# Kernel tuning notes

Hardware: AMD Instinct MI355X
Metric: run time of the kernel (lower is better)

The kernel has to match this reference:

```python
import jax, jax.numpy as jnp
import numpy as np

EMBED_DIM = 768
NUM_HEADS = 12
HEAD_DIM = EMBED_DIM // NUM_HEADS
MAX_WAVELENGTH = 10000.0
ROPE_PERCENT = 0.5


def p_rope(x, positions):
    """Partial RoPE (Gemma-style half-split layout) on x: [BH, S, D]."""
    rope_angles = int(ROPE_PERCENT * HEAD_DIM) // 2
    nope_angles = HEAD_DIM // 2 - rope_angles
    fraction = 2.0 * jnp.arange(rope_angles, dtype=x.dtype) / HEAD_DIM
    timescale = MAX_WAVELENGTH ** fraction
    # infinite timescale => angle 0 => identity rotation for the non-roped dims
    timescale = jnp.concatenate([timescale, jnp.full((nope_angles,), jnp.inf, dtype=x.dtype)])
    sinusoid = positions[:, None] / timescale[None, :]  # [S, D/2]
    sin, cos = jnp.sin(sinusoid), jnp.cos(sinusoid)
    x1, x2 = jnp.split(x, 2, axis=-1)  # each [BH, S, D/2]
    return jnp.concatenate([x1 * cos - x2 * sin, x2 * cos + x1 * sin], axis=-1)


def setup_inputs() -> dict:
    key = jax.random.key(0)
    ks = jax.random.split(key, 9)
    B, T, E = 16, 1024, EMBED_DIM
    s = 0.02
    return {
        "hidden_states": jax.random.normal(ks[0], (B, T, E), jnp.float32),
        "wq": jax.random.normal(ks[1], (E, E), jnp.float32) * s,
        "bq": jax.random.normal(ks[2], (E,), jnp.float32) * s,
        "wk": jax.random.normal(ks[3], (E, E), jnp.float32) * s,
        "bk": jax.random.normal(ks[4], (E,), jnp.float32) * s,
        "wv": jax.random.normal(ks[5], (E, E), jnp.float32) * s,
        "bv": jax.random.normal(ks[6], (E,), jnp.float32) * s,
        "wo": jax.random.normal(ks[7], (E, E), jnp.float32) * s,
        "bo": jax.random.normal(ks[8], (E,), jnp.float32) * s,
    }


def _shape(x, B, S):
    # [B, S, E] -> [B*H, S, head_dim]
    return x.reshape(B, S, NUM_HEADS, HEAD_DIM).transpose(0, 2, 1, 3).reshape(B * NUM_HEADS, S, HEAD_DIM)


def reference(hidden_states, wq, bq, wk, bk, wv, bv, wo, bo):
    B, T, E = hidden_states.shape
    scaling = HEAD_DIM ** -0.5
    # torch nn.Linear: y = x @ W.T + b
    q = (hidden_states @ wq.T + bq) * scaling
    k = hidden_states @ wk.T + bk
    v = hidden_states @ wv.T + bv
    q = _shape(q, B, T)  # [BH, T, D]
    k = _shape(k, B, T)
    v = _shape(v, B, T)
    positions = jnp.arange(T, dtype=hidden_states.dtype)
    k = p_rope(k, positions)
    q = p_rope(q, positions)
    attn = jnp.einsum('bqd,bkd->bqk', q, k)  # [BH, T, T]
    attn = jax.nn.softmax(attn, axis=-1)
    out = jnp.einsum('bqk,bkd->bqd', attn, v)  # [BH, T, D]
    out = out.reshape(B, NUM_HEADS, T, HEAD_DIM).transpose(0, 2, 1, 3).reshape(B, T, E)
    return out @ wo.T + bo
```

## Files before the change

### kernel.cpp

```cpp
#include <hip/hip_runtime.h>
#include <hip/hip_bf16.h>
#include <math.h>

typedef __hip_bfloat16 bf16;
typedef __attribute__((ext_vector_type(8))) __bf16 bf16x8;
typedef __attribute__((ext_vector_type(8))) unsigned short u16x8;
typedef __attribute__((ext_vector_type(4))) float f32x4;
typedef __attribute__((ext_vector_type(16))) float f32x16;
typedef unsigned int u32;
typedef __attribute__((ext_vector_type(4))) unsigned int u32x4;

#define DEVI static __device__ __forceinline__

#define BATCH 16
#define SEQ 1024
#define EMB 768
#define NHEAD 12
#define HDIM 64
#define BHEADS (BATCH * NHEAD)
#define MROWS (BATCH * SEQ)

DEVI f32x4 mfma16x16(bf16x8 a, bf16x8 b, f32x4 c) {
  return __builtin_amdgcn_mfma_f32_16x16x32_bf16(a, b, c, 0, 0, 0);
}
DEVI f32x16 mfma32x32(bf16x8 a, bf16x8 b, f32x16 c) {
  return __builtin_amdgcn_mfma_f32_32x32x16_bf16(a, b, c, 0, 0, 0);
}

DEVI void gload_lds16(const bf16* g, void* lds) {
  __builtin_amdgcn_global_load_lds(
      (const __attribute__((address_space(1))) void*)g,
      (__attribute__((address_space(3))) void*)lds, 16, 0, 0);
}

#if __has_builtin(__builtin_amdgcn_exp2f)
DEVI float fexp2(float x) { return __builtin_amdgcn_exp2f(x); }
#else
DEVI float fexp2(float x) { return exp2f(x); }
#endif

DEVI unsigned short f2bf_bits(float f) {
  bf16 h = __float2bfloat16(f);
  return *reinterpret_cast<unsigned short*>(&h);
}
DEVI u32 pack2(float lo, float hi) {
  return (u32)f2bf_bits(lo) | ((u32)f2bf_bits(hi) << 16);
}

#define N_HS8 (MROWS * EMB / 8)
#define N_W8 (EMB * EMB / 8)

__global__ __launch_bounds__(256) void convert_all_kernel(
    const float* __restrict__ hs, const float* __restrict__ w0,
    const float* __restrict__ w1, const float* __restrict__ w2,
    const float* __restrict__ w3, bf16* __restrict__ dhs,
    bf16* __restrict__ d0, bf16* __restrict__ d1, bf16* __restrict__ d2,
    bf16* __restrict__ d3) {
  int i = blockIdx.x * 256 + threadIdx.x;
  const float* src;
  bf16* dst;
  int j;
  if (i < N_HS8) {
    src = hs; dst = dhs; j = i;
  } else {
    int r = i - N_HS8;
    int which = r / N_W8;
    j = r - which * N_W8;
    src = (which == 0) ? w0 : (which == 1) ? w1 : (which == 2) ? w2 : w3;
    dst = (which == 0) ? d0 : (which == 1) ? d1 : (which == 2) ? d2 : d3;
  }
  const float4* s = (const float4*)src + (long)j * 2;
  float4 a = s[0], b = s[1];
  u16x8 r;
  r[0] = f2bf_bits(a.x); r[1] = f2bf_bits(a.y);
  r[2] = f2bf_bits(a.z); r[3] = f2bf_bits(a.w);
  r[4] = f2bf_bits(b.x); r[5] = f2bf_bits(b.y);
  r[6] = f2bf_bits(b.z); r[7] = f2bf_bits(b.w);
  *(u16x8*)(dst + (long)j * 8) = r;
}

__global__ void rope_table_kernel(float2* __restrict__ tbl) {
  int i = blockIdx.x * 256 + threadIdx.x;
  if (i >= SEQ * 16) return;
  int t = i >> 4;
  int d = i & 15;
  double inv_ts = pow(10000.0, -(double)d / 32.0);
  double ang = (double)t * inv_ts;
  tbl[i] = make_float2((float)cos(ang), (float)sin(ang));
}

DEVI void gemm_core_768(const bf16* __restrict__ A, const bf16* __restrict__ Bt,
                        int rowBase, int colBase, bf16* Asm, bf16* Bsm,
                        f32x4 (&acc)[4][4]) {
  const int K = 768;
  const int NT = 24;
  const int tid = threadIdx.x;
  const int wave = tid >> 6;
  const int lane = tid & 63;
  const int c0 = lane & 15;
  const int khi = lane >> 4;
  const int wm = wave >> 1, wn = wave & 1;
  const int srow = tid >> 2;
  const int scol = ((tid & 3) ^ ((tid >> 3) & 3)) * 8;
  const int sl = (khi ^ ((c0 >> 1) & 3)) * 8;
  const bf16* aG = A + (long)(rowBase + srow) * K + scol;
  const bf16* bG = Bt + (long)(colBase + srow) * K + scol;
  char* aL0 = (char*)Asm + wave * 1024;
  char* aL1 = (char*)Asm + 4096 + wave * 1024;
  char* bL0 = (char*)Bsm + wave * 1024;
  char* bL1 = (char*)Bsm + 4096 + wave * 1024;
  const int stride64 = 64 * K;

#define G_STAGE(boff, kk)                                                    \
  gload_lds16(aG + (kk), aL0 + (boff));                                      \
  gload_lds16(aG + stride64 + (kk), aL1 + (boff));                           \
  gload_lds16(bG + (kk), bL0 + (boff));                                      \
  gload_lds16(bG + stride64 + (kk), bL1 + (boff));

#define G_COMPUTE(be)                                                        \
  {                                                                          \
    bf16x8 af[4], bfr[4];                                                    \
    _Pragma("unroll") for (int m = 0; m < 4; ++m) af[m] =                    \
        *(const bf16x8*)(Asm + (be) + (wm * 64 + m * 16 + c0) * 32 + sl);    \
    _Pragma("unroll") for (int n = 0; n < 4; ++n) bfr[n] =                   \
        *(const bf16x8*)(Bsm + (be) + (wn * 64 + n * 16 + c0) * 32 + sl);    \
    __builtin_amdgcn_s_setprio(1);                                           \
    _Pragma("unroll") for (int m = 0; m < 4; ++m)                            \
      _Pragma("unroll") for (int n = 0; n < 4; ++n)                          \
        acc[m][n] = mfma16x16(af[m], bfr[n], acc[m][n]);                     \
    __builtin_amdgcn_s_setprio(0);                                           \
  }

#define G_PHASE(beElem, sByte, tc)                                           \
  {                                                                          \
    if ((tc) + 1 < NT) {                                                     \
      asm volatile("s_waitcnt vmcnt(4)" ::: "memory");                       \
    } else {                                                                 \
      asm volatile("s_waitcnt vmcnt(0)" ::: "memory");                       \
    }                                                                        \
    __builtin_amdgcn_s_barrier();                                            \
    __builtin_amdgcn_sched_barrier(0);                                       \
    if ((tc) + 2 < NT) { G_STAGE(sByte, ((tc) + 2) * 32); }                  \
    G_COMPUTE(beElem);                                                       \
  }

  G_STAGE(0, 0);
  G_STAGE(8192, 32);

  for (int tt = 0; tt < NT; tt += 3) {
    G_PHASE(0, 16384, tt);
    G_PHASE(4096, 0, tt + 1);
    G_PHASE(8192, 8192, tt + 2);
  }
#undef G_PHASE
#undef G_STAGE
#undef G_COMPUTE
}

__global__ __launch_bounds__(256, 3) void qkv_kernel(
    const bf16* __restrict__ hs,
    const bf16* __restrict__ wq, const float* __restrict__ bq,
    const bf16* __restrict__ wk, const float* __restrict__ bk,
    const bf16* __restrict__ wv, const float* __restrict__ bv,
    const float2* __restrict__ tbl,
    bf16* __restrict__ Qb, bf16* __restrict__ Kb, bf16* __restrict__ Vtb) {
  __shared__ __align__(16) bf16 Asm[3 * 128 * 32];
  __shared__ __align__(16) bf16 Bsm[3 * 128 * 32];
  const int bid = blockIdx.x;
  const int xcd = bid & 7;
  const int i = bid >> 3;
  const int rowtile = xcd * 16 + (i & 15);
  const int yz = i >> 4;
  const int type = yz % 3;
  const int coltile = yz / 3;
  const bf16* W = (type == 0) ? wq : (type == 1) ? wk : wv;
  const float* bias = (type == 0) ? bq : (type == 1) ? bk : bv;
  const int rowBase = rowtile * 128;
  const int colBase = coltile * 128;
  f32x4 acc[4][4] = {};
  gemm_core_768(hs, W, rowBase, colBase, Asm, Bsm, acc);

  const int tid = threadIdx.x;
  const int wave = tid >> 6, lane = tid & 63;
  const int c0 = lane & 15, khi = lane >> 4;
  const int wm = wave >> 1, wn = wave & 1;
  const int colW = colBase + wn * 64;
  const int head = colW >> 6;
  float bb[4];
#pragma unroll
  for (int n = 0; n < 4; ++n) bb[n] = bias[colW + n * 16 + c0];

  const int rW = rowBase + wm * 64;
  const int bIdx = rW >> 10;
  const int bh = bIdx * NHEAD + head;

  if (type == 2) {
#pragma unroll
    for (int m = 0; m < 4; ++m) {
      const int t0 = (rW & 1023) + m * 16 + khi * 4;
#pragma unroll
      for (int n = 0; n < 4; ++n) {
        const int d = n * 16 + c0;
        bf16* vp = Vtb + ((long)bh * HDIM + d) * SEQ + t0;
        ushort4 pk;
        pk.x = f2bf_bits(acc[m][n][0] + bb[n]);
        pk.y = f2bf_bits(acc[m][n][1] + bb[n]);
        pk.z = f2bf_bits(acc[m][n][2] + bb[n]);
        pk.w = f2bf_bits(acc[m][n][3] + bb[n]);
        *(ushort4*)vp = pk;
      }
    }
  } else {
    const float scl = (type == 0) ? 0.125f * 1.44269504f : 1.0f;
    bf16* base = ((type == 0) ? Qb : Kb) + (long)bh * SEQ * HDIM;
#pragma unroll
    for (int m = 0; m < 4; ++m) {
#pragma unroll
      for (int ri = 0; ri < 4; ++ri) {
        const int t = (rW & 1023) + m * 16 + khi * 4 + ri;
        float v0 = (acc[m][0][ri] + bb[0]) * scl;
        float v1 = (acc[m][1][ri] + bb[1]) * scl;
        float v2 = (acc[m][2][ri] + bb[2]) * scl;
        float v3 = (acc[m][3][ri] + bb[3]) * scl;
        const float2 cs = tbl[t * 16 + c0];
        const float r0 = v0 * cs.x - v2 * cs.y;
        const float r2 = v2 * cs.x + v0 * cs.y;
        bf16* qp = base + (long)t * HDIM;
        qp[c0] = __float2bfloat16(r0);
        qp[16 + c0] = __float2bfloat16(v1);
        qp[32 + c0] = __float2bfloat16(r2);
        qp[48 + c0] = __float2bfloat16(v3);
      }
    }
  }
}


DEVI int swoff(int row, int s) {
  return row * 128 + (((s ^ (row & 7)) & 7) << 4);
}

__global__ __launch_bounds__(256, 2) void attn_kernel(
    const bf16* __restrict__ Q, const bf16* __restrict__ K,
    const bf16* __restrict__ Vt, bf16* __restrict__ Ao) {
  __shared__ __align__(16) char smem[4 * 8192];
  const int bid = blockIdx.x;
  const int xcd = bid & 7, idx = bid >> 3;
  const int bh = xcd + ((idx >> 2) << 3);
  const int qt = idx & 3;

  const int tid = threadIdx.x;
  const int lane = tid & 63;
  const int w = tid >> 6;
  const int l31 = lane & 31;
  const int hi = lane >> 5;

  const bf16* Qh = Q + (long)bh * SEQ * HDIM;
  const bf16* Kh = K + (long)bh * SEQ * HDIM;
  const bf16* Vh = Vt + (long)bh * HDIM * SEQ;

  const int qbase = qt * 256 + w * 64;
  bf16x8 qf[2][4];
#pragma unroll
  for (int qn = 0; qn < 2; ++qn)
#pragma unroll
    for (int ks = 0; ks < 4; ++ks)
      qf[qn][ks] = *(const bf16x8*)(Qh + (qbase + qn * 32 + l31) * HDIM +
                                    ks * 16 + hi * 8);

  f32x16 o[2][2] = {};
  float lacc[2] = {0.f, 0.f};

  const int sr = tid >> 3;
  const int sc = tid & 7;

  bf16x8 kr0 = *(const bf16x8*)(Kh + sr * HDIM + sc * 8);
  bf16x8 kr1 = *(const bf16x8*)(Kh + (sr + 32) * HDIM + sc * 8);
  bf16x8 vr0 = *(const bf16x8*)(Vh + sr * SEQ + sc * 8);
  bf16x8 vr1 = *(const bf16x8*)(Vh + (sr + 32) * SEQ + sc * 8);
  *(bf16x8*)(smem + swoff(sr, sc)) = kr0;
  *(bf16x8*)(smem + swoff(sr + 32, sc)) = kr1;
  *(bf16x8*)(smem + 16384 + swoff(sr, sc)) = vr0;
  *(bf16x8*)(smem + 16384 + swoff(sr + 32, sc)) = vr1;
  __syncthreads();

  for (int ct = 0; ct < SEQ / 64; ++ct) {
    const int co = (ct & 1) * 8192;
    const char* Kc = smem + co;
    const char* Vc = smem + 16384 + co;

    if (ct != 15) {
      const int nt = (ct + 1) * 64;
      kr0 = *(const bf16x8*)(Kh + (nt + sr) * HDIM + sc * 8);
      kr1 = *(const bf16x8*)(Kh + (nt + sr + 32) * HDIM + sc * 8);
      vr0 = *(const bf16x8*)(Vh + sr * SEQ + nt + sc * 8);
      vr1 = *(const bf16x8*)(Vh + (sr + 32) * SEQ + nt + sc * 8);
    }

    f32x16 s[2][2] = {};
#pragma unroll
    for (int m = 0; m < 2; ++m)
#pragma unroll
      for (int ks = 0; ks < 4; ++ks) {
        bf16x8 ka = *(const bf16x8*)(Kc + swoff(m * 32 + l31, ks * 2 + hi));
        s[m][0] = mfma32x32(ka, qf[0][ks], s[m][0]);
        s[m][1] = mfma32x32(ka, qf[1][ks], s[m][1]);
      }

    bf16x8 pf[2][4];
#pragma unroll
    for (int qn = 0; qn < 2; ++qn) {
      u32 wds[2][4][2];
#pragma unroll
      for (int m = 0; m < 2; ++m)
#pragma unroll
        for (int b = 0; b < 4; ++b)
#pragma unroll
          for (int pp = 0; pp < 2; ++pp) {
            const float p0 = fexp2(s[m][qn][4 * b + 2 * pp]);
            const float p1 = fexp2(s[m][qn][4 * b + 2 * pp + 1]);
            lacc[qn] += p0 + p1;
            wds[m][b][pp] = pack2(p0, p1);
          }
#pragma unroll
      for (int m = 0; m < 2; ++m)
#pragma unroll
        for (int ts = 0; ts < 2; ++ts) {
          u32 x0 = wds[m][2 * ts][0], y0 = wds[m][2 * ts + 1][0];
          u32 x1 = wds[m][2 * ts][1], y1 = wds[m][2 * ts + 1][1];
          asm("v_permlane32_swap_b32 %0, %1" : "+v"(x0), "+v"(y0));
          asm("v_permlane32_swap_b32 %0, %1" : "+v"(x1), "+v"(y1));
          u32x4 t = {x0, x1, y0, y1};
          pf[qn][2 * m + ts] = *(bf16x8*)&t;
        }
    }

#pragma unroll
    for (int dm = 0; dm < 2; ++dm)
#pragma unroll
      for (int tk = 0; tk < 4; ++tk) {
        bf16x8 va = *(const bf16x8*)(Vc + swoff(dm * 32 + l31, tk * 2 + hi));
        o[dm][0] = mfma32x32(va, pf[0][tk], o[dm][0]);
        o[dm][1] = mfma32x32(va, pf[1][tk], o[dm][1]);
      }

    if (ct != 15) {
      const int no = 8192 - co;
      *(bf16x8*)(smem + no + swoff(sr, sc)) = kr0;
      *(bf16x8*)(smem + no + swoff(sr + 32, sc)) = kr1;
      *(bf16x8*)(smem + 16384 + no + swoff(sr, sc)) = vr0;
      *(bf16x8*)(smem + 16384 + no + swoff(sr + 32, sc)) = vr1;
      __syncthreads();
    }
  }

#pragma unroll
  for (int qn = 0; qn < 2; ++qn) lacc[qn] += __shfl_xor(lacc[qn], 32);
  const float inv0 = 1.0f / lacc[0];
  const float inv1 = 1.0f / lacc[1];

  const int bb = bh / NHEAD;
  const int hh = bh % NHEAD;
#pragma unroll
  for (int qn = 0; qn < 2; ++qn) {
    const float inv = qn ? inv1 : inv0;
    const int t = qbase + qn * 32 + l31;
    bf16* orow = Ao + (long)(bb * SEQ + t) * EMB + hh * HDIM;
#pragma unroll
    for (int dm = 0; dm < 2; ++dm)
#pragma unroll
      for (int b = 0; b < 4; ++b)
#pragma unroll
        for (int pp = 0; pp < 2; ++pp) {
          const int r = 4 * b + 2 * pp;
          const int d = dm * 32 + 2 * pp + 8 * b + 4 * hi;
          *(u32*)(orow + d) = pack2(o[dm][qn][r] * inv, o[dm][qn][r + 1] * inv);
        }
  }
}

__global__ __launch_bounds__(256, 3) void oproj_kernel(
    const bf16* __restrict__ X, const bf16* __restrict__ wo,
    const float* __restrict__ bo, float* __restrict__ out) {
  __shared__ __align__(16) bf16 Asm[3 * 128 * 32];
  __shared__ __align__(16) bf16 Bsm[3 * 128 * 32];
  const int bid = blockIdx.x;
  const int xcd = bid & 7;
  const int i = bid >> 3;
  const int rowBase = (xcd * 16 + (i & 15)) * 128;
  const int colBase = (i >> 4) * 128;
  f32x4 acc[4][4] = {};
  gemm_core_768(X, wo, rowBase, colBase, Asm, Bsm, acc);
  const int tid = threadIdx.x;
  const int wave = tid >> 6, lane = tid & 63;
  const int c0 = lane & 15, khi = lane >> 4;
  const int wm = wave >> 1, wn = wave & 1;
  const int colW = colBase + wn * 64;
  float bb[4];
#pragma unroll
  for (int n = 0; n < 4; ++n) bb[n] = bo[colW + n * 16 + c0];
#pragma unroll
  for (int m = 0; m < 4; ++m)
#pragma unroll
    for (int ri = 0; ri < 4; ++ri) {
      const int row = rowBase + wm * 64 + m * 16 + khi * 4 + ri;
      float* op = out + (long)row * EMB + colW;
#pragma unroll
      for (int n = 0; n < 4; ++n)
        op[n * 16 + c0] = acc[m][n][ri] + bb[n];
    }
}

extern "C" void kernel_launch(void* const* d_in, const int* in_sizes, int n_in,
                              void* d_out, int out_size, void* d_ws, size_t ws_size,
                              hipStream_t stream) {
  const float* hs_f = (const float*)d_in[0];
  const float* wq_f = (const float*)d_in[1];
  const float* bq = (const float*)d_in[2];
  const float* wk_f = (const float*)d_in[3];
  const float* bk = (const float*)d_in[4];
  const float* wv_f = (const float*)d_in[5];
  const float* bv = (const float*)d_in[6];
  const float* wo_f = (const float*)d_in[7];
  const float* bo = (const float*)d_in[8];
  float* out = (float*)d_out;

  char* ws = (char*)d_ws;
  size_t off = 0;
  float2* tbl = (float2*)ws; off += 131072;
  const size_t hsBytes = (size_t)MROWS * EMB * 2;
  const size_t wBytes = (size_t)EMB * EMB * 2;
  const size_t bufBytes = (size_t)BHEADS * SEQ * HDIM * 2;
  bf16* hsb = (bf16*)(ws + off); off += hsBytes;
  bf16* wqb = (bf16*)(ws + off); off += wBytes;
  bf16* wkb = (bf16*)(ws + off); off += wBytes;
  bf16* wvb = (bf16*)(ws + off); off += wBytes;
  bf16* wob = (bf16*)(ws + off); off += wBytes;
  bf16* Qb = (bf16*)(ws + off); off += bufBytes;
  bf16* Kb = (bf16*)(ws + off); off += bufBytes;
  bf16* Vtb = (bf16*)(ws + off); off += bufBytes;
  bf16* Ao = (bf16*)(ws + off);

  const int nConv = N_HS8 + 4 * N_W8;
  convert_all_kernel<<<dim3((nConv + 255) / 256), dim3(256), 0, stream>>>(
      hs_f, wq_f, wk_f, wv_f, wo_f, hsb, wqb, wkb, wvb, wob);
  rope_table_kernel<<<dim3(64), dim3(256), 0, stream>>>(tbl);
  qkv_kernel<<<dim3(2304), dim3(256), 0, stream>>>(
      hsb, wqb, bq, wkb, bk, wvb, bv, tbl, Qb, Kb, Vtb);
  attn_kernel<<<dim3(768), dim3(256), 0, stream>>>(Qb, Kb, Vtb, Ao);
  oproj_kernel<<<dim3(768), dim3(256), 0, stream>>>(Ao, wob, bo, out);
}
```

Measured before the change: 181.7 us.

## Fuse fp32-to-bf16 conversion of hidden states into QKV GEMM A-tile loading

Drops the standalone pass that converted the 16x1024x768 fp32 activations to bf16. The QKV GEMM now loads fp32 A tiles into registers, packs them to bf16 and writes them to LDS itself, while B tiles still use direct global-to-LDS loads. The rope-table kernel is merged into the weight-conversion launch, and the s_setprio calls around the MFMAs are removed from the shared GEMM core. This saves a full read and write of the activation tensor plus one launch, but the QKV kernel now reads twice the A bytes through registers, and each of the 6 column-tile blocks sharing a row tile repeats the conversion.

New measurement: 189.4 us. 1.04x slower.

```diff
diff --git a/kernel.cpp b/kernel.cpp
--- a/kernel.cpp
+++ b/kernel.cpp
@@ -47,46 +47,37 @@
   return (u32)f2bf_bits(lo) | ((u32)f2bf_bits(hi) << 16);
 }
 
-#define N_HS8 (MROWS * EMB / 8)
 #define N_W8 (EMB * EMB / 8)
 
-__global__ __launch_bounds__(256) void convert_all_kernel(
-    const float* __restrict__ hs, const float* __restrict__ w0,
-    const float* __restrict__ w1, const float* __restrict__ w2,
-    const float* __restrict__ w3, bf16* __restrict__ dhs,
+__global__ __launch_bounds__(256) void convert_wt_kernel(
+    const float* __restrict__ w0, const float* __restrict__ w1,
+    const float* __restrict__ w2, const float* __restrict__ w3,
     bf16* __restrict__ d0, bf16* __restrict__ d1, bf16* __restrict__ d2,
-    bf16* __restrict__ d3) {
+    bf16* __restrict__ d3, float2* __restrict__ tbl) {
   int i = blockIdx.x * 256 + threadIdx.x;
-  const float* src;
-  bf16* dst;
-  int j;
-  if (i < N_HS8) {
-    src = hs; dst = dhs; j = i;
+  if (i < 4 * N_W8) {
+    int which = i / N_W8;
+    int j = i - which * N_W8;
+    const float* src = (which == 0) ? w0 : (which == 1) ? w1
+                                       : (which == 2) ? w2 : w3;
+    bf16* dst = (which == 0) ? d0 : (which == 1) ? d1 : (which == 2) ? d2 : d3;
+    const float4* s = (const float4*)src + (long)j * 2;
+    float4 a = s[0], b = s[1];
+    u16x8 r;
+    r[0] = f2bf_bits(a.x); r[1] = f2bf_bits(a.y);
+    r[2] = f2bf_bits(a.z); r[3] = f2bf_bits(a.w);
+    r[4] = f2bf_bits(b.x); r[5] = f2bf_bits(b.y);
+    r[6] = f2bf_bits(b.z); r[7] = f2bf_bits(b.w);
+    *(u16x8*)(dst + (long)j * 8) = r;
   } else {
-    int r = i - N_HS8;
-    int which = r / N_W8;
-    j = r - which * N_W8;
-    src = (which == 0) ? w0 : (which == 1) ? w1 : (which == 2) ? w2 : w3;
-    dst = (which == 0) ? d0 : (which == 1) ? d1 : (which == 2) ? d2 : d3;
-  }
-  const float4* s = (const float4*)src + (long)j * 2;
-  float4 a = s[0], b = s[1];
-  u16x8 r;
-  r[0] = f2bf_bits(a.x); r[1] = f2bf_bits(a.y);
-  r[2] = f2bf_bits(a.z); r[3] = f2bf_bits(a.w);
-  r[4] = f2bf_bits(b.x); r[5] = f2bf_bits(b.y);
-  r[6] = f2bf_bits(b.z); r[7] = f2bf_bits(b.w);
-  *(u16x8*)(dst + (long)j * 8) = r;
-}
-
-__global__ void rope_table_kernel(float2* __restrict__ tbl) {
-  int i = blockIdx.x * 256 + threadIdx.x;
-  if (i >= SEQ * 16) return;
-  int t = i >> 4;
-  int d = i & 15;
-  double inv_ts = pow(10000.0, -(double)d / 32.0);
-  double ang = (double)t * inv_ts;
-  tbl[i] = make_float2((float)cos(ang), (float)sin(ang));
+    int e = i - 4 * N_W8;
+    if (e >= SEQ * 16) return;
+    int t = e >> 4;
+    int d = e & 15;
+    double inv_ts = pow(10000.0, -(double)d / 32.0);
+    double ang = (double)t * inv_ts;
+    tbl[e] = make_float2((float)cos(ang), (float)sin(ang));
+  }
 }
 
 DEVI void gemm_core_768(const bf16* __restrict__ A, const bf16* __restrict__ Bt,
@@ -124,11 +115,9 @@
         *(const bf16x8*)(Asm + (be) + (wm * 64 + m * 16 + c0) * 32 + sl);    \
     _Pragma("unroll") for (int n = 0; n < 4; ++n) bfr[n] =                   \
         *(const bf16x8*)(Bsm + (be) + (wn * 64 + n * 16 + c0) * 32 + sl);    \
-    __builtin_amdgcn_s_setprio(1);                                           \
     _Pragma("unroll") for (int m = 0; m < 4; ++m)                            \
       _Pragma("unroll") for (int n = 0; n < 4; ++n)                          \
         acc[m][n] = mfma16x16(af[m], bfr[n], acc[m][n]);                     \
-    __builtin_amdgcn_s_setprio(0);                                           \
   }
 
 #define G_PHASE(beElem, sByte, tc)                                           \
@@ -146,7 +135,6 @@
 
   G_STAGE(0, 0);
   G_STAGE(8192, 32);
-
   for (int tt = 0; tt < NT; tt += 3) {
     G_PHASE(0, 16384, tt);
     G_PHASE(4096, 0, tt + 1);
@@ -157,8 +145,103 @@
 #undef G_COMPUTE
 }
 
+DEVI void gemm_core_768_f32a(const float* __restrict__ Af,
+                             const bf16* __restrict__ Bt,
+                             int rowBase, int colBase, bf16* Asm, bf16* Bsm,
+                             f32x4 (&acc)[4][4]) {
+  const int K = 768;
+  const int NT = 24;
+  const int tid = threadIdx.x;
+  const int wave = tid >> 6;
+  const int lane = tid & 63;
+  const int c0 = lane & 15;
+  const int khi = lane >> 4;
+  const int wm = wave >> 1, wn = wave & 1;
+  const int srow = tid >> 2;
+  const int scol = ((tid & 3) ^ ((tid >> 3) & 3)) * 8;
+  const int sl = (khi ^ ((c0 >> 1) & 3)) * 8;
+  const float* aGf = Af + (long)(rowBase + srow) * K + scol;
+  const bf16* bG = Bt + (long)(colBase + srow) * K + scol;
+  char* aW0 = (char*)Asm + tid * 16;
+  char* aW1 = (char*)Asm + 4096 + tid * 16;
+  char* bL0 = (char*)Bsm + wave * 1024;
+  char* bL1 = (char*)Bsm + 4096 + wave * 1024;
+  const int s64 = 64 * K;
+
+  f32x4 ar00, ar01, ar10, ar11;
+
+#define GA_LOAD(kk)                                                          \
+  ar00 = *(const f32x4*)(aGf + (kk));                                        \
+  ar01 = *(const f32x4*)(aGf + (kk) + 4);                                    \
+  ar10 = *(const f32x4*)(aGf + s64 + (kk));                                  \
+  ar11 = *(const f32x4*)(aGf + s64 + (kk) + 4);
+
+#define GB_STAGE(boff, kk)                                                   \
+  gload_lds16(bG + (kk), bL0 + (boff));                                      \
+  gload_lds16(bG + s64 + (kk), bL1 + (boff));
+
+#define GA_WRITE(boff)                                                       \
+  {                                                                          \
+    u32x4 w0, w1;                                                            \
+    w0[0] = pack2(ar00[0], ar00[1]); w0[1] = pack2(ar00[2], ar00[3]);        \
+    w0[2] = pack2(ar01[0], ar01[1]); w0[3] = pack2(ar01[2], ar01[3]);        \
+    w1[0] = pack2(ar10[0], ar10[1]); w1[1] = pack2(ar10[2], ar10[3]);        \
+    w1[2] = pack2(ar11[0], ar11[1]); w1[3] = pack2(ar11[2], ar11[3]);        \
+    *(u32x4*)(aW0 + (boff)) = w0;                                            \
+    *(u32x4*)(aW1 + (boff)) = w1;                                            \
+  }
+
+#define G_COMPUTE(be)                                                        \
+  {                                                                          \
+    bf16x8 af[4], bfr[4];                                                    \
+    _Pragma("unroll") for (int m = 0; m < 4; ++m) af[m] =                    \
+        *(const bf16x8*)(Asm + (be) / 2 + (wm * 64 + m * 16 + c0) * 32 + sl);\
+    _Pragma("unroll") for (int n = 0; n < 4; ++n) bfr[n] =                   \
+        *(const bf16x8*)(Bsm + (be) / 2 + (wn * 64 + n * 16 + c0) * 32 + sl);\
+    _Pragma("unroll") for (int m = 0; m < 4; ++m)                            \
+      _Pragma("unroll") for (int n = 0; n < 4; ++n)                          \
+        acc[m][n] = mfma16x16(af[m], bfr[n], acc[m][n]);                     \
+  }
+
+#define GF_PHASE(beB, aWB, bSB, tc)                                          \
+  {                                                                          \
+    if ((tc) < NT - 1) {                                                     \
+      asm volatile("s_waitcnt vmcnt(2)" ::: "memory");                       \
+    } else {                                                                 \
+      asm volatile("s_waitcnt vmcnt(0)" ::: "memory");                       \
+    }                                                                        \
+    asm volatile("s_waitcnt lgkmcnt(0)" ::: "memory");                       \
+    __builtin_amdgcn_s_barrier();                                            \
+    __builtin_amdgcn_sched_barrier(0);                                       \
+    if ((tc) + 1 < NT) { GA_WRITE(aWB); }                                    \
+    if ((tc) + 2 < NT) {                                                     \
+      GA_LOAD(((tc) + 2) * 32);                                              \
+      GB_STAGE(bSB, ((tc) + 2) * 32);                                        \
+    }                                                                        \
+    G_COMPUTE(beB);                                                          \
+  }
+
+  GA_LOAD(0);
+  GB_STAGE(0, 0);
+  asm volatile("s_waitcnt vmcnt(2)" ::: "memory");
+  GA_WRITE(0);
+  GA_LOAD(32);
+  GB_STAGE(8192, 32);
+
+  for (int tt = 0; tt < NT; tt += 3) {
+    GF_PHASE(0, 8192, 16384, tt);
+    GF_PHASE(8192, 16384, 0, tt + 1);
+    GF_PHASE(16384, 0, 8192, tt + 2);
+  }
+#undef GF_PHASE
+#undef G_COMPUTE
+#undef GA_WRITE
+#undef GB_STAGE
+#undef GA_LOAD
+}
+
 __global__ __launch_bounds__(256, 3) void qkv_kernel(
-    const bf16* __restrict__ hs,
+    const float* __restrict__ hs,
     const bf16* __restrict__ wq, const float* __restrict__ bq,
     const bf16* __restrict__ wk, const float* __restrict__ bk,
     const bf16* __restrict__ wv, const float* __restrict__ bv,
@@ -178,7 +261,7 @@
   const int rowBase = rowtile * 128;
   const int colBase = coltile * 128;
   f32x4 acc[4][4] = {};
-  gemm_core_768(hs, W, rowBase, colBase, Asm, Bsm, acc);
+  gemm_core_768_f32a(hs, W, rowBase, colBase, Asm, Bsm, acc);
 
   const int tid = threadIdx.x;
   const int wave = tid >> 6, lane = tid & 63;
@@ -428,10 +511,8 @@
   char* ws = (char*)d_ws;
   size_t off = 0;
   float2* tbl = (float2*)ws; off += 131072;
-  const size_t hsBytes = (size_t)MROWS * EMB * 2;
   const size_t wBytes = (size_t)EMB * EMB * 2;
   const size_t bufBytes = (size_t)BHEADS * SEQ * HDIM * 2;
-  bf16* hsb = (bf16*)(ws + off); off += hsBytes;
   bf16* wqb = (bf16*)(ws + off); off += wBytes;
   bf16* wkb = (bf16*)(ws + off); off += wBytes;
   bf16* wvb = (bf16*)(ws + off); off += wBytes;
@@ -441,12 +522,11 @@
   bf16* Vtb = (bf16*)(ws + off); off += bufBytes;
   bf16* Ao = (bf16*)(ws + off);
 
-  const int nConv = N_HS8 + 4 * N_W8;
-  convert_all_kernel<<<dim3((nConv + 255) / 256), dim3(256), 0, stream>>>(
-      hs_f, wq_f, wk_f, wv_f, wo_f, hsb, wqb, wkb, wvb, wob);
-  rope_table_kernel<<<dim3(64), dim3(256), 0, stream>>>(tbl);
+  const int nConv = 4 * N_W8 + SEQ * 16;
+  convert_wt_kernel<<<dim3((nConv + 255) / 256), dim3(256), 0, stream>>>(
+      wq_f, wk_f, wv_f, wo_f, wqb, wkb, wvb, wob, tbl);
   qkv_kernel<<<dim3(2304), dim3(256), 0, stream>>>(
-      hsb, wqb, bq, wkb, bk, wvb, bv, tbl, Qb, Kb, Vtb);
+      hs_f, wqb, bq, wkb, bk, wvb, bv, tbl, Qb, Kb, Vtb);
   attn_kernel<<<dim3(768), dim3(256), 0, stream>>>(Qb, Kb, Vtb, Ao);
   oproj_kernel<<<dim3(768), dim3(256), 0, stream>>>(Ao, wob, bo, out);
 }
```
